# Performance work log

Measured on AMD Instinct MI355X. Metric: run time of the kernel, lower is better.

## Reference

```python
import jax, jax.numpy as jnp
from jax import lax
import numpy as np

SLOPE = 0.1  # LeakyReLU negative slope used throughout DA_conv


def setup_inputs() -> dict:
    key = jax.random.key(0)
    ks = jax.random.split(key, 8)
    B, C, H, W = 16, 64, 160, 160
    Cout, red = 64, 8
    feat = jax.random.normal(ks[0], (B, C, H, W), dtype=jnp.float32)
    deg = jax.random.normal(ks[1], (B, C, 1, 1), dtype=jnp.float32)
    W1 = jax.random.normal(ks[2], (64, C), dtype=jnp.float32) * 0.05
    W2 = jax.random.normal(ks[3], (Cout * 9, 64), dtype=jnp.float32) * 0.05
    Wc = jax.random.normal(ks[4], (Cout, Cout), dtype=jnp.float32) * 0.05
    bc = jnp.zeros((Cout,), dtype=jnp.float32)
    Wd1 = jax.random.normal(ks[5], (red, C), dtype=jnp.float32) * 0.05
    Wd2 = jax.random.normal(ks[6], (Cout, red), dtype=jnp.float32) * 0.05
    return {"feat": feat, "deg": deg, "W1": W1, "W2": W2, "Wc": Wc,
            "bc": bc, "Wd1": Wd1, "Wd2": Wd2}


def reference(feat, deg, W1, W2, Wc, bc, Wd1, Wd2):
    B, C, H, W = feat.shape
    Cout = Wc.shape[0]
    KS = 3
    d = deg[:, :, 0, 0]  # [B, C]

    # --- dynamic per-sample, per-channel 3x3 kernel generation ---
    h = jax.nn.leaky_relu(d @ W1.T, SLOPE)            # [B, 64]
    k = (h @ W2.T).reshape(B * Cout, 1, KS, KS)        # [B*Cout, 1, 3, 3]

    # grouped depthwise conv: input [1, B*C, H, W], groups = B*C
    x = feat.reshape(1, B * C, H, W)
    out = lax.conv_general_dilated(
        x, k, window_strides=(1, 1), padding=[(1, 1), (1, 1)],
        dimension_numbers=("NCHW", "OIHW", "NCHW"),
        feature_group_count=B * C)
    out = jax.nn.leaky_relu(out, SLOPE).reshape(B, Cout, H, W)

    # 1x1 conv with bias (common.default_conv)
    out = jnp.einsum("oi,bihw->bohw", Wc, out) + bc[None, :, None, None]

    # --- channel attention branch (1x1 convs == matmuls on [B,C]) ---
    a = jax.nn.leaky_relu(jnp.einsum("ri,bi->br", Wd1, d), SLOPE)   # [B, red]
    att = jax.nn.sigmoid(jnp.einsum("or,br->bo", Wd2, a))           # [B, Cout]

    return out + feat * att[:, :, None, None]
```

## Files before the change

kernel.cpp:

```cpp
#include <hip/hip_runtime.h>
#include <hip/hip_bf16.h>
#include <math.h>

#define SLOPE 0.1f
#define B_ 16
#define C_ 64
#define H_ 160
#define W_ 160
#define HW_ (H_*W_)

typedef short bf16x8 __attribute__((ext_vector_type(8)));
typedef float f32x4  __attribute__((ext_vector_type(4)));
typedef unsigned int uint2v __attribute__((ext_vector_type(2)));

__device__ __forceinline__ float lrelu(float x) { return fmaxf(x, SLOPE * x); }
__device__ __forceinline__ unsigned f2bf(float x) {
  union { float f; unsigned u; } c; c.f = x;
  return (c.u + 0x7fffu + ((c.u >> 16) & 1u)) >> 16;
}
__device__ __forceinline__ float bf2f(unsigned short u) {
  union { unsigned u; float f; } c; c.u = ((unsigned)u) << 16; return c.f;
}

__device__ __forceinline__ void gl2lds16(const void* g, void* l) {
  __builtin_amdgcn_global_load_lds(
      (const __attribute__((address_space(1))) void*)g,
      (__attribute__((address_space(3))) void*)l, 16, 0, 0);
}

__global__ __launch_bounds__(64) void prep_kernel(
    const float* __restrict__ deg,
    const float* __restrict__ W1,
    const float* __restrict__ W2,
    const float* __restrict__ Wd1,
    const float* __restrict__ Wd2,
    float* __restrict__ ws) {
  const int b = blockIdx.x;
  const int j = threadIdx.x;
  __shared__ float sd[64], sh[64], sa[8];
  sd[j] = deg[b * 64 + j];
  __syncthreads();

  float acc = 0.f;
  for (int i = 0; i < 64; ++i) acc = fmaf(sd[i], W1[j * 64 + i], acc);
  sh[j] = lrelu(acc);

  if (j < 8) {
    float s = 0.f;
    for (int i = 0; i < 64; ++i) s = fmaf(sd[i], Wd1[j * 64 + i], s);
    sa[j] = lrelu(s);
  }
  __syncthreads();

  float kv[9];
#pragma unroll
  for (int t = 0; t < 9; ++t) kv[t] = 0.f;
  for (int l = 0; l < 64; ++l) {
    float hl = sh[l];
#pragma unroll
    for (int t = 0; t < 9; ++t) kv[t] = fmaf(hl, W2[(j * 9 + t) * 64 + l], kv[t]);
  }
  unsigned short* kw = (unsigned short*)(ws + 1024) + (b * 64 + j) * 16;
#pragma unroll
  for (int t = 0; t < 9; ++t) kw[t] = (unsigned short)f2bf(kv[t]);
#pragma unroll
  for (int t = 9; t < 16; ++t) kw[t] = 0;

  float s2 = 0.f;
#pragma unroll
  for (int r = 0; r < 8; ++r) s2 = fmaf(Wd2[j * 8 + r], sa[r], s2);
  ws[b * 64 + j] = 1.f / (1.f + __expf(-s2));
}

__global__ __launch_bounds__(256, 4) void main_kernel(
    const float* __restrict__ feat,
    const float* __restrict__ Wc,
    const float* __restrict__ bc,
    const float* __restrict__ ws,
    float* __restrict__ out) {
  __shared__ __align__(16) float S[2][16][240];
  __shared__ __align__(16) unsigned short Tt[2048];
  __shared__ __align__(16) unsigned short Ff[2048];
  __shared__ __align__(16) unsigned short Kl[1024];

  const int rb  = blockIdx.x;
  const int bid = (rb & 7) * 400 + (rb >> 3);
  const int b   = bid / 200;
  const int rem = bid - b * 200;
  const int ty  = rem / 10, tx = rem - ty * 10;
  const int x0 = tx * 16, y0 = ty * 8;
  const int tid = threadIdx.x;
  const int lane = tid & 63, wid = tid >> 6;

  const float* __restrict__ attp  = ws + b * 64;
  const char*  __restrict__ kb8   = (const char*)(ws + 1024) + b * 2048;
  const float* __restrict__ plane = feat + (size_t)(b * 64) * HW_;

  const int ci = tid >> 4;
  const int q  = (tid >> 2) & 3;
  const int h  = tid & 3;
  const int nl = lane & 15, kg = lane >> 4;
  const int ochunk = wid * 16;

  const int srow = lane / 6;
  const int schk = lane - srow * 6;
  const int grow = min(max(y0 + srow - 1, 0), H_ - 1);
  const int gcol = min(max(x0 - 4 + schk * 4, 0), W_ - 4);
  const float* sp0 = plane + grow * W_ + gcol;

  union AF { bf16x8 v; unsigned short u[8]; };
  AF a[4];
#pragma unroll
  for (int g = 0; g < 4; ++g) {
    const float4 w = *(const float4*)(Wc + (ochunk + nl) * 64 + g * 16 + 4 * kg);
    a[g].u[0] = (unsigned short)f2bf(w.x); a[g].u[1] = (unsigned short)f2bf(w.y);
    a[g].u[2] = (unsigned short)f2bf(w.z); a[g].u[3] = (unsigned short)f2bf(w.w);
    a[g].u[4] = 0; a[g].u[5] = 0; a[g].u[6] = 0; a[g].u[7] = 0;
  }
  AF a2;
  {
    const unsigned short ab = (unsigned short)f2bf(attp[ochunk + nl]);
#pragma unroll
    for (int j = 0; j < 4; ++j) a2.u[j] = (nl == 4 * kg + j) ? ab : (unsigned short)0;
    a2.u[4] = 0; a2.u[5] = 0; a2.u[6] = 0; a2.u[7] = 0;
  }
  const float4 bcv = *(const float4*)(bc + ochunk + 4 * kg);

  asm volatile("s_waitcnt vmcnt(0)" ::: "memory");

  if (wid == 0) {
    gl2lds16(kb8 + lane * 16, &Kl[0]);
    gl2lds16(kb8 + 1024 + lane * 16, &Kl[512]);
  }
#define STAGE(g_, bf_) \
  if (lane < 60) { \
    const float* s_ = sp0 + (size_t)((g_) * 16 + wid * 4) * HW_; \
    gl2lds16(s_,            &S[bf_][wid * 4 + 0][0]); \
    gl2lds16(s_ + HW_,      &S[bf_][wid * 4 + 1][0]); \
    gl2lds16(s_ + 2 * HW_,  &S[bf_][wid * 4 + 2][0]); \
    gl2lds16(s_ + 3 * HW_,  &S[bf_][wid * 4 + 3][0]); \
  }
  STAGE(0, 0);
  asm volatile("s_waitcnt vmcnt(4)" ::: "memory");
  __builtin_amdgcn_s_barrier();
  __builtin_amdgcn_sched_barrier(0);

  f32x4 acc[8];
#pragma unroll
  for (int nt = 0; nt < 8; ++nt) acc[nt] = (f32x4){0.f, 0.f, 0.f, 0.f};

  const float mlz = (x0 == 0 && q == 0) ? 0.f : 1.f;
  const float mrz = (x0 == W_ - 16 && q == 3) ? 0.f : 1.f;

  const unsigned t_base = (unsigned)(uintptr_t)&Tt[0] + (unsigned)(lane * 8);
  const unsigned f_base = (unsigned)(uintptr_t)&Ff[0] + (unsigned)(lane * 8);
  union BU { bf16x8 v; uint2v qv[2]; };

#pragma unroll
  for (int g = 0; g < 4; ++g) {
    const int sb = g & 1;
    if (g < 3) {
      STAGE(g + 1, (g + 1) & 1);
      asm volatile("s_waitcnt vmcnt(4)" ::: "memory");
    } else {
      asm volatile("s_waitcnt vmcnt(0)" ::: "memory");
    }
    __builtin_amdgcn_sched_barrier(0);

    const unsigned short* kr = &Kl[(g * 16 + ci) * 16];
    union KU { uint4 v; unsigned short u[8]; } k07;
    k07.v = *(const uint4*)kr;
    const unsigned short k8u = kr[8];
    float kk[9];
#pragma unroll
    for (int t = 0; t < 8; ++t) kk[t] = bf2f(k07.u[t]);
    kk[8] = bf2f(k8u);

    float rv[4][9];
#pragma unroll
    for (int rr = 0; rr < 4; ++rr) {
      const float* sp = &S[sb][ci][(2 * h + rr) * 24 + 4 * q];
      const f32x4 v0 = *(const f32x4*)sp;
      const f32x4 v1 = *(const f32x4*)(sp + 4);
      rv[rr][0] = v0[0]; rv[rr][1] = v0[1]; rv[rr][2] = v0[2];
      rv[rr][3] = v0[3] * mlz;
      rv[rr][4] = v1[0]; rv[rr][5] = v1[1]; rv[rr][6] = v1[2]; rv[rr][7] = v1[3];
      rv[rr][8] = sp[8] * mrz;
    }

#pragma unroll
    for (int rr = 0; rr < 2; ++rr) {
      const int srw = 2 * h + rr;
      const float mt = (srw == 0 && y0 == 0) ? 0.f : 1.f;
      const float mb = (srw == 7 && y0 == H_ - 8) ? 0.f : 1.f;
      float sv[4], fv[4];
#pragma unroll
      for (int j = 0; j < 4; ++j) {
        float ts = fmaf(rv[rr][j + 5], kk[2], fmaf(rv[rr][j + 4], kk[1], rv[rr][j + 3] * kk[0]));
        float cs = fmaf(rv[rr + 1][j + 5], kk[5], fmaf(rv[rr + 1][j + 4], kk[4], rv[rr + 1][j + 3] * kk[3]));
        float bs = fmaf(rv[rr + 2][j + 5], kk[8], fmaf(rv[rr + 2][j + 4], kk[7], rv[rr + 2][j + 3] * kk[6]));
        sv[j] = fmaf(mt, ts, fmaf(mb, bs, cs));
        fv[j] = rv[rr + 1][j + 4];
      }
      uint2v tq, fq;
      tq.x = f2bf(lrelu(sv[0])) | (f2bf(lrelu(sv[1])) << 16);
      tq.y = f2bf(lrelu(sv[2])) | (f2bf(lrelu(sv[3])) << 16);
      fq.x = f2bf(fv[0]) | (f2bf(fv[1]) << 16);
      fq.y = f2bf(fv[2]) | (f2bf(fv[3]) << 16);
      const int tidx = srw * 256 + ci * 16 + 4 * q;
      *(uint2v*)&Tt[tidx] = tq;
      *(uint2v*)&Ff[tidx] = fq;
    }

    asm volatile("s_waitcnt lgkmcnt(0)" ::: "memory");
    __builtin_amdgcn_sched_barrier(0);
    __builtin_amdgcn_s_barrier();
    __builtin_amdgcn_sched_barrier(0);

    uint2v ta0, ta1, ta2, ta3, tb0, tb1, tb2, tb3;
    asm volatile("ds_read_b64_tr_b16 %0, %1 offset:0"    : "=v"(ta0) : "v"(t_base));
    asm volatile("ds_read_b64_tr_b16 %0, %1 offset:512"  : "=v"(ta1) : "v"(t_base));
    asm volatile("ds_read_b64_tr_b16 %0, %1 offset:1024" : "=v"(ta2) : "v"(t_base));
    asm volatile("ds_read_b64_tr_b16 %0, %1 offset:1536" : "=v"(ta3) : "v"(t_base));
    asm volatile("s_waitcnt lgkmcnt(0)" ::: "memory");
    __builtin_amdgcn_sched_barrier(0);
    asm volatile("ds_read_b64_tr_b16 %0, %1 offset:2048" : "=v"(tb0) : "v"(t_base));
    asm volatile("ds_read_b64_tr_b16 %0, %1 offset:2560" : "=v"(tb1) : "v"(t_base));
    asm volatile("ds_read_b64_tr_b16 %0, %1 offset:3072" : "=v"(tb2) : "v"(t_base));
    asm volatile("ds_read_b64_tr_b16 %0, %1 offset:3584" : "=v"(tb3) : "v"(t_base));
    {
      BU u0, u1, u2, u3;
      u0.qv[0] = ta0; u0.qv[1] = (uint2v){0u, 0u};
      u1.qv[0] = ta1; u1.qv[1] = (uint2v){0u, 0u};
      u2.qv[0] = ta2; u2.qv[1] = (uint2v){0u, 0u};
      u3.qv[0] = ta3; u3.qv[1] = (uint2v){0u, 0u};
      acc[0] = __builtin_amdgcn_mfma_f32_16x16x32_bf16(a[g].v, u0.v, acc[0], 0, 0, 0);
      acc[1] = __builtin_amdgcn_mfma_f32_16x16x32_bf16(a[g].v, u1.v, acc[1], 0, 0, 0);
      acc[2] = __builtin_amdgcn_mfma_f32_16x16x32_bf16(a[g].v, u2.v, acc[2], 0, 0, 0);
      acc[3] = __builtin_amdgcn_mfma_f32_16x16x32_bf16(a[g].v, u3.v, acc[3], 0, 0, 0);
    }
    asm volatile("s_waitcnt lgkmcnt(0)" ::: "memory");
    __builtin_amdgcn_sched_barrier(0);
    {
      BU u4, u5, u6, u7;
      u4.qv[0] = tb0; u4.qv[1] = (uint2v){0u, 0u};
      u5.qv[0] = tb1; u5.qv[1] = (uint2v){0u, 0u};
      u6.qv[0] = tb2; u6.qv[1] = (uint2v){0u, 0u};
      u7.qv[0] = tb3; u7.qv[1] = (uint2v){0u, 0u};
      acc[4] = __builtin_amdgcn_mfma_f32_16x16x32_bf16(a[g].v, u4.v, acc[4], 0, 0, 0);
      acc[5] = __builtin_amdgcn_mfma_f32_16x16x32_bf16(a[g].v, u5.v, acc[5], 0, 0, 0);
      acc[6] = __builtin_amdgcn_mfma_f32_16x16x32_bf16(a[g].v, u6.v, acc[6], 0, 0, 0);
      acc[7] = __builtin_amdgcn_mfma_f32_16x16x32_bf16(a[g].v, u7.v, acc[7], 0, 0, 0);
    }
    if (wid == g) {
      uint2v fa0, fa1, fa2, fa3, fb0, fb1, fb2, fb3;
      asm volatile("ds_read_b64_tr_b16 %0, %1 offset:0"    : "=v"(fa0) : "v"(f_base));
      asm volatile("ds_read_b64_tr_b16 %0, %1 offset:512"  : "=v"(fa1) : "v"(f_base));
      asm volatile("ds_read_b64_tr_b16 %0, %1 offset:1024" : "=v"(fa2) : "v"(f_base));
      asm volatile("ds_read_b64_tr_b16 %0, %1 offset:1536" : "=v"(fa3) : "v"(f_base));
      asm volatile("s_waitcnt lgkmcnt(0)" ::: "memory");
      __builtin_amdgcn_sched_barrier(0);
      asm volatile("ds_read_b64_tr_b16 %0, %1 offset:2048" : "=v"(fb0) : "v"(f_base));
      asm volatile("ds_read_b64_tr_b16 %0, %1 offset:2560" : "=v"(fb1) : "v"(f_base));
      asm volatile("ds_read_b64_tr_b16 %0, %1 offset:3072" : "=v"(fb2) : "v"(f_base));
      asm volatile("ds_read_b64_tr_b16 %0, %1 offset:3584" : "=v"(fb3) : "v"(f_base));
      {
        BU u0, u1, u2, u3;
        u0.qv[0] = fa0; u0.qv[1] = (uint2v){0u, 0u};
        u1.qv[0] = fa1; u1.qv[1] = (uint2v){0u, 0u};
        u2.qv[0] = fa2; u2.qv[1] = (uint2v){0u, 0u};
        u3.qv[0] = fa3; u3.qv[1] = (uint2v){0u, 0u};
        acc[0] = __builtin_amdgcn_mfma_f32_16x16x32_bf16(a2.v, u0.v, acc[0], 0, 0, 0);
        acc[1] = __builtin_amdgcn_mfma_f32_16x16x32_bf16(a2.v, u1.v, acc[1], 0, 0, 0);
        acc[2] = __builtin_amdgcn_mfma_f32_16x16x32_bf16(a2.v, u2.v, acc[2], 0, 0, 0);
        acc[3] = __builtin_amdgcn_mfma_f32_16x16x32_bf16(a2.v, u3.v, acc[3], 0, 0, 0);
      }
      asm volatile("s_waitcnt lgkmcnt(0)" ::: "memory");
      __builtin_amdgcn_sched_barrier(0);
      {
        BU u4, u5, u6, u7;
        u4.qv[0] = fb0; u4.qv[1] = (uint2v){0u, 0u};
        u5.qv[0] = fb1; u5.qv[1] = (uint2v){0u, 0u};
        u6.qv[0] = fb2; u6.qv[1] = (uint2v){0u, 0u};
        u7.qv[0] = fb3; u7.qv[1] = (uint2v){0u, 0u};
        acc[4] = __builtin_amdgcn_mfma_f32_16x16x32_bf16(a2.v, u4.v, acc[4], 0, 0, 0);
        acc[5] = __builtin_amdgcn_mfma_f32_16x16x32_bf16(a2.v, u5.v, acc[5], 0, 0, 0);
        acc[6] = __builtin_amdgcn_mfma_f32_16x16x32_bf16(a2.v, u6.v, acc[6], 0, 0, 0);
        acc[7] = __builtin_amdgcn_mfma_f32_16x16x32_bf16(a2.v, u7.v, acc[7], 0, 0, 0);
      }
    }
    __builtin_amdgcn_s_barrier();
    __builtin_amdgcn_sched_barrier(0);
  }
#undef STAGE

  const int ob = ochunk + 4 * kg;
  float* __restrict__ outb = out + (size_t)(b * 64) * HW_;
#pragma unroll
  for (int nt = 0; nt < 8; ++nt) {
    const int off = (y0 + nt) * W_ + x0 + nl;
    outb[(size_t)(ob + 0) * HW_ + off] = acc[nt][0] + bcv.x;
    outb[(size_t)(ob + 1) * HW_ + off] = acc[nt][1] + bcv.y;
    outb[(size_t)(ob + 2) * HW_ + off] = acc[nt][2] + bcv.z;
    outb[(size_t)(ob + 3) * HW_ + off] = acc[nt][3] + bcv.w;
  }
}

extern "C" void kernel_launch(void* const* d_in, const int* in_sizes, int n_in,
                              void* d_out, int out_size, void* d_ws, size_t ws_size,
                              hipStream_t stream) {
  const float* feat = (const float*)d_in[0];
  const float* deg  = (const float*)d_in[1];
  const float* W1   = (const float*)d_in[2];
  const float* W2   = (const float*)d_in[3];
  const float* Wc   = (const float*)d_in[4];
  const float* bc   = (const float*)d_in[5];
  const float* Wd1  = (const float*)d_in[6];
  const float* Wd2  = (const float*)d_in[7];
  float* out = (float*)d_out;
  float* ws  = (float*)d_ws;

  prep_kernel<<<dim3(B_), dim3(64), 0, stream>>>(deg, W1, W2, Wd1, Wd2, ws);
  main_kernel<<<dim3(3200), dim3(256), 0, stream>>>(feat, Wc, bc, ws, out);
}
```

Measured before the change: 67.30 us.

## Move attention residual to fp32 epilogue and double-buffer the transpose LDS tile

Drops the bf16 staging of feat into LDS and the extra attention-diagonal MFMA pass. The residual feat*att is now added in the epilogue by re-reading feat from global memory in fp32. The T tile is double-buffered by stage parity, which removes the trailing per-group barrier. This saves LDS writes, transposed reads, MFMAs and one barrier per group, at the cost of an extra global read of feat per output element (likely cache hits) and relying on parity buffering for correctness.

```diff
diff --git a/kernel.cpp b/kernel.cpp
--- a/kernel.cpp
+++ b/kernel.cpp
@@ -79,8 +79,7 @@
     const float* __restrict__ ws,
     float* __restrict__ out) {
   __shared__ __align__(16) float S[2][16][240];
-  __shared__ __align__(16) unsigned short Tt[2048];
-  __shared__ __align__(16) unsigned short Ff[2048];
+  __shared__ __align__(16) unsigned short Tt[4096];
   __shared__ __align__(16) unsigned short Kl[1024];
 
   const int rb  = blockIdx.x;
@@ -117,14 +116,8 @@
     a[g].u[2] = (unsigned short)f2bf(w.z); a[g].u[3] = (unsigned short)f2bf(w.w);
     a[g].u[4] = 0; a[g].u[5] = 0; a[g].u[6] = 0; a[g].u[7] = 0;
   }
-  AF a2;
-  {
-    const unsigned short ab = (unsigned short)f2bf(attp[ochunk + nl]);
-#pragma unroll
-    for (int j = 0; j < 4; ++j) a2.u[j] = (nl == 4 * kg + j) ? ab : (unsigned short)0;
-    a2.u[4] = 0; a2.u[5] = 0; a2.u[6] = 0; a2.u[7] = 0;
-  }
   const float4 bcv = *(const float4*)(bc + ochunk + 4 * kg);
+  const float4 atv = *(const float4*)(attp + ochunk + 4 * kg);
 
   asm volatile("s_waitcnt vmcnt(0)" ::: "memory");
 
@@ -153,7 +146,6 @@
   const float mrz = (x0 == W_ - 16 && q == 3) ? 0.f : 1.f;
 
   const unsigned t_base = (unsigned)(uintptr_t)&Tt[0] + (unsigned)(lane * 8);
-  const unsigned f_base = (unsigned)(uintptr_t)&Ff[0] + (unsigned)(lane * 8);
   union BU { bf16x8 v; uint2v qv[2]; };
 
 #pragma unroll
@@ -193,23 +185,18 @@
       const int srw = 2 * h + rr;
       const float mt = (srw == 0 && y0 == 0) ? 0.f : 1.f;
       const float mb = (srw == 7 && y0 == H_ - 8) ? 0.f : 1.f;
-      float sv[4], fv[4];
+      float sv[4];
 #pragma unroll
       for (int j = 0; j < 4; ++j) {
         float ts = fmaf(rv[rr][j + 5], kk[2], fmaf(rv[rr][j + 4], kk[1], rv[rr][j + 3] * kk[0]));
         float cs = fmaf(rv[rr + 1][j + 5], kk[5], fmaf(rv[rr + 1][j + 4], kk[4], rv[rr + 1][j + 3] * kk[3]));
         float bs = fmaf(rv[rr + 2][j + 5], kk[8], fmaf(rv[rr + 2][j + 4], kk[7], rv[rr + 2][j + 3] * kk[6]));
         sv[j] = fmaf(mt, ts, fmaf(mb, bs, cs));
-        fv[j] = rv[rr + 1][j + 4];
       }
-      uint2v tq, fq;
+      uint2v tq;
       tq.x = f2bf(lrelu(sv[0])) | (f2bf(lrelu(sv[1])) << 16);
       tq.y = f2bf(lrelu(sv[2])) | (f2bf(lrelu(sv[3])) << 16);
-      fq.x = f2bf(fv[0]) | (f2bf(fv[1]) << 16);
-      fq.y = f2bf(fv[2]) | (f2bf(fv[3]) << 16);
-      const int tidx = srw * 256 + ci * 16 + 4 * q;
-      *(uint2v*)&Tt[tidx] = tq;
-      *(uint2v*)&Ff[tidx] = fq;
+      *(uint2v*)&Tt[sb * 2048 + srw * 256 + ci * 16 + 4 * q] = tq;
     }
 
     asm volatile("s_waitcnt lgkmcnt(0)" ::: "memory");
@@ -217,17 +204,18 @@
     __builtin_amdgcn_s_barrier();
     __builtin_amdgcn_sched_barrier(0);
 
+    const unsigned tb = t_base + (unsigned)(sb * 4096);
     uint2v ta0, ta1, ta2, ta3, tb0, tb1, tb2, tb3;
-    asm volatile("ds_read_b64_tr_b16 %0, %1 offset:0"    : "=v"(ta0) : "v"(t_base));
-    asm volatile("ds_read_b64_tr_b16 %0, %1 offset:512"  : "=v"(ta1) : "v"(t_base));
-    asm volatile("ds_read_b64_tr_b16 %0, %1 offset:1024" : "=v"(ta2) : "v"(t_base));
-    asm volatile("ds_read_b64_tr_b16 %0, %1 offset:1536" : "=v"(ta3) : "v"(t_base));
+    asm volatile("ds_read_b64_tr_b16 %0, %1 offset:0"    : "=v"(ta0) : "v"(tb));
+    asm volatile("ds_read_b64_tr_b16 %0, %1 offset:512"  : "=v"(ta1) : "v"(tb));
+    asm volatile("ds_read_b64_tr_b16 %0, %1 offset:1024" : "=v"(ta2) : "v"(tb));
+    asm volatile("ds_read_b64_tr_b16 %0, %1 offset:1536" : "=v"(ta3) : "v"(tb));
     asm volatile("s_waitcnt lgkmcnt(0)" ::: "memory");
     __builtin_amdgcn_sched_barrier(0);
-    asm volatile("ds_read_b64_tr_b16 %0, %1 offset:2048" : "=v"(tb0) : "v"(t_base));
-    asm volatile("ds_read_b64_tr_b16 %0, %1 offset:2560" : "=v"(tb1) : "v"(t_base));
-    asm volatile("ds_read_b64_tr_b16 %0, %1 offset:3072" : "=v"(tb2) : "v"(t_base));
-    asm volatile("ds_read_b64_tr_b16 %0, %1 offset:3584" : "=v"(tb3) : "v"(t_base));
+    asm volatile("ds_read_b64_tr_b16 %0, %1 offset:2048" : "=v"(tb0) : "v"(tb));
+    asm volatile("ds_read_b64_tr_b16 %0, %1 offset:2560" : "=v"(tb1) : "v"(tb));
+    asm volatile("ds_read_b64_tr_b16 %0, %1 offset:3072" : "=v"(tb2) : "v"(tb));
+    asm volatile("ds_read_b64_tr_b16 %0, %1 offset:3584" : "=v"(tb3) : "v"(tb));
     {
       BU u0, u1, u2, u3;
       u0.qv[0] = ta0; u0.qv[1] = (uint2v){0u, 0u};
@@ -252,57 +240,32 @@
       acc[6] = __builtin_amdgcn_mfma_f32_16x16x32_bf16(a[g].v, u6.v, acc[6], 0, 0, 0);
       acc[7] = __builtin_amdgcn_mfma_f32_16x16x32_bf16(a[g].v, u7.v, acc[7], 0, 0, 0);
     }
-    if (wid == g) {
-      uint2v fa0, fa1, fa2, fa3, fb0, fb1, fb2, fb3;
-      asm volatile("ds_read_b64_tr_b16 %0, %1 offset:0"    : "=v"(fa0) : "v"(f_base));
-      asm volatile("ds_read_b64_tr_b16 %0, %1 offset:512"  : "=v"(fa1) : "v"(f_base));
-      asm volatile("ds_read_b64_tr_b16 %0, %1 offset:1024" : "=v"(fa2) : "v"(f_base));
-      asm volatile("ds_read_b64_tr_b16 %0, %1 offset:1536" : "=v"(fa3) : "v"(f_base));
-      asm volatile("s_waitcnt lgkmcnt(0)" ::: "memory");
-      __builtin_amdgcn_sched_barrier(0);
-      asm volatile("ds_read_b64_tr_b16 %0, %1 offset:2048" : "=v"(fb0) : "v"(f_base));
-      asm volatile("ds_read_b64_tr_b16 %0, %1 offset:2560" : "=v"(fb1) : "v"(f_base));
-      asm volatile("ds_read_b64_tr_b16 %0, %1 offset:3072" : "=v"(fb2) : "v"(f_base));
-      asm volatile("ds_read_b64_tr_b16 %0, %1 offset:3584" : "=v"(fb3) : "v"(f_base));
-      {
-        BU u0, u1, u2, u3;
-        u0.qv[0] = fa0; u0.qv[1] = (uint2v){0u, 0u};
-        u1.qv[0] = fa1; u1.qv[1] = (uint2v){0u, 0u};
-        u2.qv[0] = fa2; u2.qv[1] = (uint2v){0u, 0u};
-        u3.qv[0] = fa3; u3.qv[1] = (uint2v){0u, 0u};
-        acc[0] = __builtin_amdgcn_mfma_f32_16x16x32_bf16(a2.v, u0.v, acc[0], 0, 0, 0);
-        acc[1] = __builtin_amdgcn_mfma_f32_16x16x32_bf16(a2.v, u1.v, acc[1], 0, 0, 0);
-        acc[2] = __builtin_amdgcn_mfma_f32_16x16x32_bf16(a2.v, u2.v, acc[2], 0, 0, 0);
-        acc[3] = __builtin_amdgcn_mfma_f32_16x16x32_bf16(a2.v, u3.v, acc[3], 0, 0, 0);
-      }
-      asm volatile("s_waitcnt lgkmcnt(0)" ::: "memory");
-      __builtin_amdgcn_sched_barrier(0);
-      {
-        BU u4, u5, u6, u7;
-        u4.qv[0] = fb0; u4.qv[1] = (uint2v){0u, 0u};
-        u5.qv[0] = fb1; u5.qv[1] = (uint2v){0u, 0u};
-        u6.qv[0] = fb2; u6.qv[1] = (uint2v){0u, 0u};
-        u7.qv[0] = fb3; u7.qv[1] = (uint2v){0u, 0u};
-        acc[4] = __builtin_amdgcn_mfma_f32_16x16x32_bf16(a2.v, u4.v, acc[4], 0, 0, 0);
-        acc[5] = __builtin_amdgcn_mfma_f32_16x16x32_bf16(a2.v, u5.v, acc[5], 0, 0, 0);
-        acc[6] = __builtin_amdgcn_mfma_f32_16x16x32_bf16(a2.v, u6.v, acc[6], 0, 0, 0);
-        acc[7] = __builtin_amdgcn_mfma_f32_16x16x32_bf16(a2.v, u7.v, acc[7], 0, 0, 0);
-      }
-    }
-    __builtin_amdgcn_s_barrier();
-    __builtin_amdgcn_sched_barrier(0);
   }
 #undef STAGE
 
   const int ob = ochunk + 4 * kg;
-  float* __restrict__ outb = out + (size_t)(b * 64) * HW_;
-#pragma unroll
-  for (int nt = 0; nt < 8; ++nt) {
-    const int off = (y0 + nt) * W_ + x0 + nl;
-    outb[(size_t)(ob + 0) * HW_ + off] = acc[nt][0] + bcv.x;
-    outb[(size_t)(ob + 1) * HW_ + off] = acc[nt][1] + bcv.y;
-    outb[(size_t)(ob + 2) * HW_ + off] = acc[nt][2] + bcv.z;
-    outb[(size_t)(ob + 3) * HW_ + off] = acc[nt][3] + bcv.w;
+  const float* __restrict__ rbase = plane + (size_t)ob * HW_ + y0 * W_ + x0 + nl;
+  float* __restrict__ outb = out + (size_t)(b * 64 + ob) * HW_ + y0 * W_ + x0 + nl;
+
+#pragma unroll
+  for (int half = 0; half < 2; ++half) {
+    float fr[4][4];
+#pragma unroll
+    for (int i = 0; i < 4; ++i) {
+      const int nt = half * 4 + i;
+#pragma unroll
+      for (int j = 0; j < 4; ++j)
+        fr[i][j] = rbase[(size_t)j * HW_ + nt * W_];
+    }
+#pragma unroll
+    for (int i = 0; i < 4; ++i) {
+      const int nt = half * 4 + i;
+#pragma unroll
+      for (int j = 0; j < 4; ++j)
+        outb[(size_t)j * HW_ + nt * W_] =
+            fmaf(fr[i][j], ((const float*)&atv)[j],
+                 acc[nt][j] + ((const float*)&bcv)[j]);
+    }
   }
 }
 
```

Measured after the change: 72.31 us. 1.07x slower.

## Process four tiles per block with cross-tile prefetch of first channel stage

Applied to the files above, without the earlier changes.

The grid shrinks from 3200 to 800 blocks. Each block now loops over four consecutive spatial tiles of the same batch image. Weight conversion, attention setup and the dynamic-kernel LDS load are done once per block instead of once per tile. During the last channel group of each tile, the first channel group of the next tile is prefetched into the free LDS buffer, so the global-load latency at tile boundaries overlaps with compute. The trade-off is fewer resident blocks (800 fit under a single wave of occupancy slots), which reduces latency hiding across blocks and may leave some CUs underused.

```diff
diff --git a/kernel.cpp b/kernel.cpp
--- a/kernel.cpp
+++ b/kernel.cpp
@@ -84,11 +84,9 @@
   __shared__ __align__(16) unsigned short Kl[1024];
 
   const int rb  = blockIdx.x;
-  const int bid = (rb & 7) * 400 + (rb >> 3);
-  const int b   = bid / 200;
-  const int rem = bid - b * 200;
-  const int ty  = rem / 10, tx = rem - ty * 10;
-  const int x0 = tx * 16, y0 = ty * 8;
+  const int swz = (rb & 7) * 100 + (rb >> 3);
+  const int b   = swz / 50;
+  const int s4  = (swz - b * 50) * 4;
   const int tid = threadIdx.x;
   const int lane = tid & 63, wid = tid >> 6;
 
@@ -104,9 +102,6 @@
 
   const int srow = lane / 6;
   const int schk = lane - srow * 6;
-  const int grow = min(max(y0 + srow - 1, 0), H_ - 1);
-  const int gcol = min(max(x0 - 4 + schk * 4, 0), W_ - 4);
-  const float* sp0 = plane + grow * W_ + gcol;
 
   union AF { bf16x8 v; unsigned short u[8]; };
   AF a[4];
@@ -128,182 +123,208 @@
 
   asm volatile("s_waitcnt vmcnt(0)" ::: "memory");
 
-  if (wid == 0) {
-    gl2lds16(kb8 + lane * 16, &Kl[0]);
-    gl2lds16(kb8 + 1024 + lane * 16, &Kl[512]);
-  }
-#define STAGE(g_, bf_) \
+#define STAGE(base_, g_, bf_) \
   if (lane < 60) { \
-    const float* s_ = sp0 + (size_t)((g_) * 16 + wid * 4) * HW_; \
+    const float* s_ = (base_) + (size_t)((g_) * 16 + wid * 4) * HW_; \
     gl2lds16(s_,            &S[bf_][wid * 4 + 0][0]); \
     gl2lds16(s_ + HW_,      &S[bf_][wid * 4 + 1][0]); \
     gl2lds16(s_ + 2 * HW_,  &S[bf_][wid * 4 + 2][0]); \
     gl2lds16(s_ + 3 * HW_,  &S[bf_][wid * 4 + 3][0]); \
   }
-  STAGE(0, 0);
+
+  if (wid == 0) {
+    gl2lds16(kb8 + lane * 16, &Kl[0]);
+    gl2lds16(kb8 + 1024 + lane * 16, &Kl[512]);
+  }
+  {
+    const int tl0 = s4;
+    const int ty0 = tl0 / 10, tx0 = tl0 - ty0 * 10;
+    const int y00 = ty0 * 8, x00 = tx0 * 16;
+    const int grow0 = min(max(y00 + srow - 1, 0), H_ - 1);
+    const int gcol0 = min(max(x00 - 4 + schk * 4, 0), W_ - 4);
+    const float* sp00 = plane + grow0 * W_ + gcol0;
+    STAGE(sp00, 0, 0);
+  }
   asm volatile("s_waitcnt vmcnt(4)" ::: "memory");
   __builtin_amdgcn_s_barrier();
   __builtin_amdgcn_sched_barrier(0);
 
-  f32x4 acc[8];
-#pragma unroll
-  for (int nt = 0; nt < 8; ++nt) acc[nt] = (f32x4){0.f, 0.f, 0.f, 0.f};
-
-  const float mlz = (x0 == 0 && q == 0) ? 0.f : 1.f;
-  const float mrz = (x0 == W_ - 16 && q == 3) ? 0.f : 1.f;
-
   const unsigned t_base = (unsigned)(uintptr_t)&Tt[0] + (unsigned)(lane * 8);
   const unsigned f_base = (unsigned)(uintptr_t)&Ff[0] + (unsigned)(lane * 8);
   union BU { bf16x8 v; uint2v qv[2]; };
 
-#pragma unroll
-  for (int g = 0; g < 4; ++g) {
-    const int sb = g & 1;
-    if (g < 3) {
-      STAGE(g + 1, (g + 1) & 1);
-      asm volatile("s_waitcnt vmcnt(4)" ::: "memory");
-    } else {
-      asm volatile("s_waitcnt vmcnt(0)" ::: "memory");
-    }
-    __builtin_amdgcn_sched_barrier(0);
-
-    const unsigned short* kr = &Kl[(g * 16 + ci) * 16];
-    union KU { uint4 v; unsigned short u[8]; } k07;
-    k07.v = *(const uint4*)kr;
-    const unsigned short k8u = kr[8];
-    float kk[9];
-#pragma unroll
-    for (int t = 0; t < 8; ++t) kk[t] = bf2f(k07.u[t]);
-    kk[8] = bf2f(k8u);
-
-    float rv[4][9];
-#pragma unroll
-    for (int rr = 0; rr < 4; ++rr) {
-      const float* sp = &S[sb][ci][(2 * h + rr) * 24 + 4 * q];
-      const f32x4 v0 = *(const f32x4*)sp;
-      const f32x4 v1 = *(const f32x4*)(sp + 4);
-      rv[rr][0] = v0[0]; rv[rr][1] = v0[1]; rv[rr][2] = v0[2];
-      rv[rr][3] = v0[3] * mlz;
-      rv[rr][4] = v1[0]; rv[rr][5] = v1[1]; rv[rr][6] = v1[2]; rv[rr][7] = v1[3];
-      rv[rr][8] = sp[8] * mrz;
-    }
-
-#pragma unroll
-    for (int rr = 0; rr < 2; ++rr) {
-      const int srw = 2 * h + rr;
-      const float mt = (srw == 0 && y0 == 0) ? 0.f : 1.f;
-      const float mb = (srw == 7 && y0 == H_ - 8) ? 0.f : 1.f;
-      float sv[4], fv[4];
-#pragma unroll
-      for (int j = 0; j < 4; ++j) {
-        float ts = fmaf(rv[rr][j + 5], kk[2], fmaf(rv[rr][j + 4], kk[1], rv[rr][j + 3] * kk[0]));
-        float cs = fmaf(rv[rr + 1][j + 5], kk[5], fmaf(rv[rr + 1][j + 4], kk[4], rv[rr + 1][j + 3] * kk[3]));
-        float bs = fmaf(rv[rr + 2][j + 5], kk[8], fmaf(rv[rr + 2][j + 4], kk[7], rv[rr + 2][j + 3] * kk[6]));
-        sv[j] = fmaf(mt, ts, fmaf(mb, bs, cs));
-        fv[j] = rv[rr + 1][j + 4];
-      }
-      uint2v tq, fq;
-      tq.x = f2bf(lrelu(sv[0])) | (f2bf(lrelu(sv[1])) << 16);
-      tq.y = f2bf(lrelu(sv[2])) | (f2bf(lrelu(sv[3])) << 16);
-      fq.x = f2bf(fv[0]) | (f2bf(fv[1]) << 16);
-      fq.y = f2bf(fv[2]) | (f2bf(fv[3]) << 16);
-      const int tidx = srw * 256 + ci * 16 + 4 * q;
-      *(uint2v*)&Tt[tidx] = tq;
-      *(uint2v*)&Ff[tidx] = fq;
-    }
-
-    asm volatile("s_waitcnt lgkmcnt(0)" ::: "memory");
-    __builtin_amdgcn_sched_barrier(0);
-    __builtin_amdgcn_s_barrier();
-    __builtin_amdgcn_sched_barrier(0);
-
-    uint2v ta0, ta1, ta2, ta3, tb0, tb1, tb2, tb3;
-    asm volatile("ds_read_b64_tr_b16 %0, %1 offset:0"    : "=v"(ta0) : "v"(t_base));
-    asm volatile("ds_read_b64_tr_b16 %0, %1 offset:512"  : "=v"(ta1) : "v"(t_base));
-    asm volatile("ds_read_b64_tr_b16 %0, %1 offset:1024" : "=v"(ta2) : "v"(t_base));
-    asm volatile("ds_read_b64_tr_b16 %0, %1 offset:1536" : "=v"(ta3) : "v"(t_base));
-    asm volatile("s_waitcnt lgkmcnt(0)" ::: "memory");
-    __builtin_amdgcn_sched_barrier(0);
-    asm volatile("ds_read_b64_tr_b16 %0, %1 offset:2048" : "=v"(tb0) : "v"(t_base));
-    asm volatile("ds_read_b64_tr_b16 %0, %1 offset:2560" : "=v"(tb1) : "v"(t_base));
-    asm volatile("ds_read_b64_tr_b16 %0, %1 offset:3072" : "=v"(tb2) : "v"(t_base));
-    asm volatile("ds_read_b64_tr_b16 %0, %1 offset:3584" : "=v"(tb3) : "v"(t_base));
-    {
-      BU u0, u1, u2, u3;
-      u0.qv[0] = ta0; u0.qv[1] = (uint2v){0u, 0u};
-      u1.qv[0] = ta1; u1.qv[1] = (uint2v){0u, 0u};
-      u2.qv[0] = ta2; u2.qv[1] = (uint2v){0u, 0u};
-      u3.qv[0] = ta3; u3.qv[1] = (uint2v){0u, 0u};
-      acc[0] = __builtin_amdgcn_mfma_f32_16x16x32_bf16(a[g].v, u0.v, acc[0], 0, 0, 0);
-      acc[1] = __builtin_amdgcn_mfma_f32_16x16x32_bf16(a[g].v, u1.v, acc[1], 0, 0, 0);
-      acc[2] = __builtin_amdgcn_mfma_f32_16x16x32_bf16(a[g].v, u2.v, acc[2], 0, 0, 0);
-      acc[3] = __builtin_amdgcn_mfma_f32_16x16x32_bf16(a[g].v, u3.v, acc[3], 0, 0, 0);
-    }
-    asm volatile("s_waitcnt lgkmcnt(0)" ::: "memory");
-    __builtin_amdgcn_sched_barrier(0);
-    {
-      BU u4, u5, u6, u7;
-      u4.qv[0] = tb0; u4.qv[1] = (uint2v){0u, 0u};
-      u5.qv[0] = tb1; u5.qv[1] = (uint2v){0u, 0u};
-      u6.qv[0] = tb2; u6.qv[1] = (uint2v){0u, 0u};
-      u7.qv[0] = tb3; u7.qv[1] = (uint2v){0u, 0u};
-      acc[4] = __builtin_amdgcn_mfma_f32_16x16x32_bf16(a[g].v, u4.v, acc[4], 0, 0, 0);
-      acc[5] = __builtin_amdgcn_mfma_f32_16x16x32_bf16(a[g].v, u5.v, acc[5], 0, 0, 0);
-      acc[6] = __builtin_amdgcn_mfma_f32_16x16x32_bf16(a[g].v, u6.v, acc[6], 0, 0, 0);
-      acc[7] = __builtin_amdgcn_mfma_f32_16x16x32_bf16(a[g].v, u7.v, acc[7], 0, 0, 0);
-    }
-    if (wid == g) {
-      uint2v fa0, fa1, fa2, fa3, fb0, fb1, fb2, fb3;
-      asm volatile("ds_read_b64_tr_b16 %0, %1 offset:0"    : "=v"(fa0) : "v"(f_base));
-      asm volatile("ds_read_b64_tr_b16 %0, %1 offset:512"  : "=v"(fa1) : "v"(f_base));
-      asm volatile("ds_read_b64_tr_b16 %0, %1 offset:1024" : "=v"(fa2) : "v"(f_base));
-      asm volatile("ds_read_b64_tr_b16 %0, %1 offset:1536" : "=v"(fa3) : "v"(f_base));
+#pragma unroll 1
+  for (int it = 0; it < 4; ++it) {
+    const int tl = s4 + it;
+    const int ty = tl / 10, tx = tl - ty * 10;
+    const int y0 = ty * 8, x0 = tx * 16;
+    const int grow = min(max(y0 + srow - 1, 0), H_ - 1);
+    const int gcol = min(max(x0 - 4 + schk * 4, 0), W_ - 4);
+    const float* sp0 = plane + grow * W_ + gcol;
+    const float mlz = (x0 == 0 && q == 0) ? 0.f : 1.f;
+    const float mrz = (x0 == W_ - 16 && q == 3) ? 0.f : 1.f;
+
+    f32x4 acc[8];
+#pragma unroll
+    for (int nt = 0; nt < 8; ++nt) acc[nt] = (f32x4){0.f, 0.f, 0.f, 0.f};
+
+#pragma unroll
+    for (int g = 0; g < 4; ++g) {
+      const int sb = g & 1;
+      if (g < 3) {
+        STAGE(sp0, g + 1, (g + 1) & 1);
+        asm volatile("s_waitcnt vmcnt(4)" ::: "memory");
+      } else if (it < 3) {
+        const int tl2 = tl + 1;
+        const int ty2 = tl2 / 10, tx2 = tl2 - ty2 * 10;
+        const int grow2 = min(max(ty2 * 8 + srow - 1, 0), H_ - 1);
+        const int gcol2 = min(max(tx2 * 16 - 4 + schk * 4, 0), W_ - 4);
+        const float* sp0n = plane + grow2 * W_ + gcol2;
+        STAGE(sp0n, 0, 0);
+        asm volatile("s_waitcnt vmcnt(4)" ::: "memory");
+      } else {
+        asm volatile("s_waitcnt vmcnt(0)" ::: "memory");
+      }
+      __builtin_amdgcn_sched_barrier(0);
+
+      const unsigned short* kr = &Kl[(g * 16 + ci) * 16];
+      union KU { uint4 v; unsigned short u[8]; } k07;
+      k07.v = *(const uint4*)kr;
+      const unsigned short k8u = kr[8];
+      float kk[9];
+#pragma unroll
+      for (int t = 0; t < 8; ++t) kk[t] = bf2f(k07.u[t]);
+      kk[8] = bf2f(k8u);
+
+      float rv[4][9];
+#pragma unroll
+      for (int rr = 0; rr < 4; ++rr) {
+        const float* sp = &S[sb][ci][(2 * h + rr) * 24 + 4 * q];
+        const f32x4 v0 = *(const f32x4*)sp;
+        const f32x4 v1 = *(const f32x4*)(sp + 4);
+        rv[rr][0] = v0[0]; rv[rr][1] = v0[1]; rv[rr][2] = v0[2];
+        rv[rr][3] = v0[3] * mlz;
+        rv[rr][4] = v1[0]; rv[rr][5] = v1[1]; rv[rr][6] = v1[2]; rv[rr][7] = v1[3];
+        rv[rr][8] = sp[8] * mrz;
+      }
+
+#pragma unroll
+      for (int rr = 0; rr < 2; ++rr) {
+        const int srw = 2 * h + rr;
+        const float mt = (srw == 0 && y0 == 0) ? 0.f : 1.f;
+        const float mb = (srw == 7 && y0 == H_ - 8) ? 0.f : 1.f;
+        float sv[4], fv[4];
+#pragma unroll
+        for (int j = 0; j < 4; ++j) {
+          float ts = fmaf(rv[rr][j + 5], kk[2], fmaf(rv[rr][j + 4], kk[1], rv[rr][j + 3] * kk[0]));
+          float cs = fmaf(rv[rr + 1][j + 5], kk[5], fmaf(rv[rr + 1][j + 4], kk[4], rv[rr + 1][j + 3] * kk[3]));
+          float bs = fmaf(rv[rr + 2][j + 5], kk[8], fmaf(rv[rr + 2][j + 4], kk[7], rv[rr + 2][j + 3] * kk[6]));
+          sv[j] = fmaf(mt, ts, fmaf(mb, bs, cs));
+          fv[j] = rv[rr + 1][j + 4];
+        }
+        uint2v tq, fq;
+        tq.x = f2bf(lrelu(sv[0])) | (f2bf(lrelu(sv[1])) << 16);
+        tq.y = f2bf(lrelu(sv[2])) | (f2bf(lrelu(sv[3])) << 16);
+        fq.x = f2bf(fv[0]) | (f2bf(fv[1]) << 16);
+        fq.y = f2bf(fv[2]) | (f2bf(fv[3]) << 16);
+        const int tidx = srw * 256 + ci * 16 + 4 * q;
+        *(uint2v*)&Tt[tidx] = tq;
+        *(uint2v*)&Ff[tidx] = fq;
+      }
+
       asm volatile("s_waitcnt lgkmcnt(0)" ::: "memory");
       __builtin_amdgcn_sched_barrier(0);
-      asm volatile("ds_read_b64_tr_b16 %0, %1 offset:2048" : "=v"(fb0) : "v"(f_base));
-      asm volatile("ds_read_b64_tr_b16 %0, %1 offset:2560" : "=v"(fb1) : "v"(f_base));
-      asm volatile("ds_read_b64_tr_b16 %0, %1 offset:3072" : "=v"(fb2) : "v"(f_base));
-      asm volatile("ds_read_b64_tr_b16 %0, %1 offset:3584" : "=v"(fb3) : "v"(f_base));
+      __builtin_amdgcn_s_barrier();
+      __builtin_amdgcn_sched_barrier(0);
+
+      uint2v ta0, ta1, ta2, ta3, tb0, tb1, tb2, tb3;
+      asm volatile("ds_read_b64_tr_b16 %0, %1 offset:0"    : "=v"(ta0) : "v"(t_base));
+      asm volatile("ds_read_b64_tr_b16 %0, %1 offset:512"  : "=v"(ta1) : "v"(t_base));
+      asm volatile("ds_read_b64_tr_b16 %0, %1 offset:1024" : "=v"(ta2) : "v"(t_base));
+      asm volatile("ds_read_b64_tr_b16 %0, %1 offset:1536" : "=v"(ta3) : "v"(t_base));
+      asm volatile("s_waitcnt lgkmcnt(0)" ::: "memory");
+      __builtin_amdgcn_sched_barrier(0);
+      asm volatile("ds_read_b64_tr_b16 %0, %1 offset:2048" : "=v"(tb0) : "v"(t_base));
+      asm volatile("ds_read_b64_tr_b16 %0, %1 offset:2560" : "=v"(tb1) : "v"(t_base));
+      asm volatile("ds_read_b64_tr_b16 %0, %1 offset:3072" : "=v"(tb2) : "v"(t_base));
+      asm volatile("ds_read_b64_tr_b16 %0, %1 offset:3584" : "=v"(tb3) : "v"(t_base));
       {
         BU u0, u1, u2, u3;
-        u0.qv[0] = fa0; u0.qv[1] = (uint2v){0u, 0u};
-        u1.qv[0] = fa1; u1.qv[1] = (uint2v){0u, 0u};
-        u2.qv[0] = fa2; u2.qv[1] = (uint2v){0u, 0u};
-        u3.qv[0] = fa3; u3.qv[1] = (uint2v){0u, 0u};
-        acc[0] = __builtin_amdgcn_mfma_f32_16x16x32_bf16(a2.v, u0.v, acc[0], 0, 0, 0);
-        acc[1] = __builtin_amdgcn_mfma_f32_16x16x32_bf16(a2.v, u1.v, acc[1], 0, 0, 0);
-        acc[2] = __builtin_amdgcn_mfma_f32_16x16x32_bf16(a2.v, u2.v, acc[2], 0, 0, 0);
-        acc[3] = __builtin_amdgcn_mfma_f32_16x16x32_bf16(a2.v, u3.v, acc[3], 0, 0, 0);
+        u0.qv[0] = ta0; u0.qv[1] = (uint2v){0u, 0u};
+        u1.qv[0] = ta1; u1.qv[1] = (uint2v){0u, 0u};
+        u2.qv[0] = ta2; u2.qv[1] = (uint2v){0u, 0u};
+        u3.qv[0] = ta3; u3.qv[1] = (uint2v){0u, 0u};
+        acc[0] = __builtin_amdgcn_mfma_f32_16x16x32_bf16(a[g].v, u0.v, acc[0], 0, 0, 0);
+        acc[1] = __builtin_amdgcn_mfma_f32_16x16x32_bf16(a[g].v, u1.v, acc[1], 0, 0, 0);
+        acc[2] = __builtin_amdgcn_mfma_f32_16x16x32_bf16(a[g].v, u2.v, acc[2], 0, 0, 0);
+        acc[3] = __builtin_amdgcn_mfma_f32_16x16x32_bf16(a[g].v, u3.v, acc[3], 0, 0, 0);
       }
       asm volatile("s_waitcnt lgkmcnt(0)" ::: "memory");
       __builtin_amdgcn_sched_barrier(0);
       {
         BU u4, u5, u6, u7;
-        u4.qv[0] = fb0; u4.qv[1] = (uint2v){0u, 0u};
-        u5.qv[0] = fb1; u5.qv[1] = (uint2v){0u, 0u};
-        u6.qv[0] = fb2; u6.qv[1] = (uint2v){0u, 0u};
-        u7.qv[0] = fb3; u7.qv[1] = (uint2v){0u, 0u};
-        acc[4] = __builtin_amdgcn_mfma_f32_16x16x32_bf16(a2.v, u4.v, acc[4], 0, 0, 0);
-        acc[5] = __builtin_amdgcn_mfma_f32_16x16x32_bf16(a2.v, u5.v, acc[5], 0, 0, 0);
-        acc[6] = __builtin_amdgcn_mfma_f32_16x16x32_bf16(a2.v, u6.v, acc[6], 0, 0, 0);
-        acc[7] = __builtin_amdgcn_mfma_f32_16x16x32_bf16(a2.v, u7.v, acc[7], 0, 0, 0);
-      }
+        u4.qv[0] = tb0; u4.qv[1] = (uint2v){0u, 0u};
+        u5.qv[0] = tb1; u5.qv[1] = (uint2v){0u, 0u};
+        u6.qv[0] = tb2; u6.qv[1] = (uint2v){0u, 0u};
+        u7.qv[0] = tb3; u7.qv[1] = (uint2v){0u, 0u};
+        acc[4] = __builtin_amdgcn_mfma_f32_16x16x32_bf16(a[g].v, u4.v, acc[4], 0, 0, 0);
+        acc[5] = __builtin_amdgcn_mfma_f32_16x16x32_bf16(a[g].v, u5.v, acc[5], 0, 0, 0);
+        acc[6] = __builtin_amdgcn_mfma_f32_16x16x32_bf16(a[g].v, u6.v, acc[6], 0, 0, 0);
+        acc[7] = __builtin_amdgcn_mfma_f32_16x16x32_bf16(a[g].v, u7.v, acc[7], 0, 0, 0);
+      }
+      if (wid == g) {
+        uint2v fa0, fa1, fa2, fa3, fb0, fb1, fb2, fb3;
+        asm volatile("ds_read_b64_tr_b16 %0, %1 offset:0"    : "=v"(fa0) : "v"(f_base));
+        asm volatile("ds_read_b64_tr_b16 %0, %1 offset:512"  : "=v"(fa1) : "v"(f_base));
+        asm volatile("ds_read_b64_tr_b16 %0, %1 offset:1024" : "=v"(fa2) : "v"(f_base));
+        asm volatile("ds_read_b64_tr_b16 %0, %1 offset:1536" : "=v"(fa3) : "v"(f_base));
+        asm volatile("s_waitcnt lgkmcnt(0)" ::: "memory");
+        __builtin_amdgcn_sched_barrier(0);
+        asm volatile("ds_read_b64_tr_b16 %0, %1 offset:2048" : "=v"(fb0) : "v"(f_base));
+        asm volatile("ds_read_b64_tr_b16 %0, %1 offset:2560" : "=v"(fb1) : "v"(f_base));
+        asm volatile("ds_read_b64_tr_b16 %0, %1 offset:3072" : "=v"(fb2) : "v"(f_base));
+        asm volatile("ds_read_b64_tr_b16 %0, %1 offset:3584" : "=v"(fb3) : "v"(f_base));
+        {
+          BU u0, u1, u2, u3;
+          u0.qv[0] = fa0; u0.qv[1] = (uint2v){0u, 0u};
+          u1.qv[0] = fa1; u1.qv[1] = (uint2v){0u, 0u};
+          u2.qv[0] = fa2; u2.qv[1] = (uint2v){0u, 0u};
+          u3.qv[0] = fa3; u3.qv[1] = (uint2v){0u, 0u};
+          acc[0] = __builtin_amdgcn_mfma_f32_16x16x32_bf16(a2.v, u0.v, acc[0], 0, 0, 0);
+          acc[1] = __builtin_amdgcn_mfma_f32_16x16x32_bf16(a2.v, u1.v, acc[1], 0, 0, 0);
+          acc[2] = __builtin_amdgcn_mfma_f32_16x16x32_bf16(a2.v, u2.v, acc[2], 0, 0, 0);
+          acc[3] = __builtin_amdgcn_mfma_f32_16x16x32_bf16(a2.v, u3.v, acc[3], 0, 0, 0);
+        }
+        asm volatile("s_waitcnt lgkmcnt(0)" ::: "memory");
+        __builtin_amdgcn_sched_barrier(0);
+        {
+          BU u4, u5, u6, u7;
+          u4.qv[0] = fb0; u4.qv[1] = (uint2v){0u, 0u};
+          u5.qv[0] = fb1; u5.qv[1] = (uint2v){0u, 0u};
+          u6.qv[0] = fb2; u6.qv[1] = (uint2v){0u, 0u};
+          u7.qv[0] = fb3; u7.qv[1] = (uint2v){0u, 0u};
+          acc[4] = __builtin_amdgcn_mfma_f32_16x16x32_bf16(a2.v, u4.v, acc[4], 0, 0, 0);
+          acc[5] = __builtin_amdgcn_mfma_f32_16x16x32_bf16(a2.v, u5.v, acc[5], 0, 0, 0);
+          acc[6] = __builtin_amdgcn_mfma_f32_16x16x32_bf16(a2.v, u6.v, acc[6], 0, 0, 0);
+          acc[7] = __builtin_amdgcn_mfma_f32_16x16x32_bf16(a2.v, u7.v, acc[7], 0, 0, 0);
+        }
+      }
+      __builtin_amdgcn_s_barrier();
+      __builtin_amdgcn_sched_barrier(0);
     }
-    __builtin_amdgcn_s_barrier();
-    __builtin_amdgcn_sched_barrier(0);
+
+    const int ob = ochunk + 4 * kg;
+    float* __restrict__ outb = out + (size_t)(b * 64) * HW_;
+#pragma unroll
+    for (int nt = 0; nt < 8; ++nt) {
+      const int off = (y0 + nt) * W_ + x0 + nl;
+      outb[(size_t)(ob + 0) * HW_ + off] = acc[nt][0] + bcv.x;
+      outb[(size_t)(ob + 1) * HW_ + off] = acc[nt][1] + bcv.y;
+      outb[(size_t)(ob + 2) * HW_ + off] = acc[nt][2] + bcv.z;
+      outb[(size_t)(ob + 3) * HW_ + off] = acc[nt][3] + bcv.w;
+    }
   }
 #undef STAGE
-
-  const int ob = ochunk + 4 * kg;
-  float* __restrict__ outb = out + (size_t)(b * 64) * HW_;
-#pragma unroll
-  for (int nt = 0; nt < 8; ++nt) {
-    const int off = (y0 + nt) * W_ + x0 + nl;
-    outb[(size_t)(ob + 0) * HW_ + off] = acc[nt][0] + bcv.x;
-    outb[(size_t)(ob + 1) * HW_ + off] = acc[nt][1] + bcv.y;
-    outb[(size_t)(ob + 2) * HW_ + off] = acc[nt][2] + bcv.z;
-    outb[(size_t)(ob + 3) * HW_ + off] = acc[nt][3] + bcv.w;
-  }
 }
 
 extern "C" void kernel_launch(void* const* d_in, const int* in_sizes, int n_in,
@@ -321,5 +342,5 @@
   float* ws  = (float*)d_ws;
 
   prep_kernel<<<dim3(B_), dim3(64), 0, stream>>>(deg, W1, W2, Wd1, Wd2, ws);
-  main_kernel<<<dim3(3200), dim3(256), 0, stream>>>(feat, Wc, bc, ws, out);
-}
+  main_kernel<<<dim3(800), dim3(256), 0, stream>>>(feat, Wc, bc, ws, out);
+}
```

Result: slower. 108.6 us (+61.4%).
